# Kernel tuning notes

Hardware: AMD Instinct MI355X
Metric: run time of the kernel (lower is better)

The kernel has to match this reference:

```python
import jax, jax.numpy as jnp
import numpy as np

N_NODES = 15
K = 5
L_IN = 1920
C_OUT = 256
L3 = L_IN - 3 * K + 3  # 1908
EPS = 1e-5


def setup_inputs() -> dict:
    key = jax.random.key(0)
    ks = jax.random.split(key, 18)
    B, E = 128, 56
    s = 0.05
    inp = {
        'X': jax.random.normal(ks[0], (B, N_NODES, L_IN), jnp.float32),
        'edge_index': jax.random.randint(ks[1], (2, E), 0, N_NODES),
        'edge_weight': jax.random.uniform(ks[2], (E,), jnp.float32),
        # grouped conv params (groups = N_NODES): per-group channels 1->16->32->1
        'conv1_w': jax.random.normal(ks[3], (16 * N_NODES, 1, K), jnp.float32) * s,
        'conv1_b': jnp.zeros((16 * N_NODES,), jnp.float32),
        'conv2_w': jax.random.normal(ks[4], (32 * N_NODES, 16, K), jnp.float32) * s,
        'conv2_b': jnp.zeros((32 * N_NODES,), jnp.float32),
        'conv3_w': jax.random.normal(ks[5], (N_NODES, 32, K), jnp.float32) * s,
        'conv3_b': jnp.zeros((N_NODES,), jnp.float32),
        # GCNConv: lin weight [out,in] + bias
        'gcn_w': jax.random.normal(ks[6], (C_OUT, L3), jnp.float32) * s,
        'gcn_b': jnp.zeros((C_OUT,), jnp.float32),
        'lin1_w': jax.random.normal(ks[7], (C_OUT, L_IN), jnp.float32) * s,
        'lin1_b': jnp.zeros((C_OUT,), jnp.float32),
        # GraphNorm params
        'gn_w': jnp.ones((C_OUT,), jnp.float32),
        'gn_b': jnp.zeros((C_OUT,), jnp.float32),
        'gn_ms': jnp.ones((C_OUT,), jnp.float32),
        'out_w': jax.random.normal(ks[8], (16, C_OUT), jnp.float32) * s,
        'out_b': jnp.zeros((16,), jnp.float32),
    }
    return inp


def _gconv(x, w, b):
    # grouped valid conv1d, NCH layout
    y = jax.lax.conv_general_dilated(
        x, w, window_strides=(1,), padding='VALID',
        dimension_numbers=('NCH', 'OIH', 'NCH'),
        feature_group_count=N_NODES)
    return y + b[None, :, None]


def _gcn(x, edge_index, edge_weight, W, b):
    # x: [B, N, L3]; batched GCNConv with shared edge structure (no per-t loop)
    src, dst = edge_index[0], edge_index[1]
    loop = jnp.arange(N_NODES)
    src = jnp.concatenate([src, loop])
    dst = jnp.concatenate([dst, loop])
    ew = jnp.concatenate([edge_weight, jnp.ones((N_NODES,), edge_weight.dtype)])
    deg = jnp.zeros((N_NODES,), ew.dtype).at[dst].add(ew)  # in-degree on target
    dinv = jnp.where(deg > 0, jax.lax.rsqrt(deg), 0.0)
    norm = dinv[src] * ew * dinv[dst]  # [E']
    xl = jnp.einsum('bnf,of->bno', x, W)  # [B, N, C_OUT]
    msg = norm[None, :, None] * xl[:, src, :]  # [B, E', C_OUT]
    out = jnp.zeros_like(xl).at[:, dst, :].add(msg)
    return out + b


def reference(X, edge_index, edge_weight, conv1_w, conv1_b, conv2_w, conv2_b,
              conv3_w, conv3_b, gcn_w, gcn_b, lin1_w, lin1_b, gn_w, gn_b,
              gn_ms, out_w, out_b):
    h = jax.nn.leaky_relu(_gconv(X, conv1_w, conv1_b), 0.01)
    h = jax.nn.leaky_relu(_gconv(h, conv2_w, conv2_b), 0.01)
    h = jax.nn.leaky_relu(_gconv(h, conv3_w, conv3_b), 0.01)  # [B, N, L3]
    T = _gcn(h, edge_index, edge_weight, gcn_w, gcn_b)  # [B, N, C_OUT]
    # GraphNorm with batch=None -> single graph over dim 0
    mean = T.mean(axis=0, keepdims=True)
    out = T - mean * gn_ms
    var = (out * out).mean(axis=0, keepdims=True)
    T = gn_w * out / jnp.sqrt(var + EPS) + gn_b
    T = jax.nn.elu(T + jnp.einsum('bnl,ol->bno', X, lin1_w) + lin1_b)
    output = T.mean(axis=1)  # global_mean_pool over nodes -> [B, C_OUT]
    class_output = output @ out_w.T + out_b  # [B, 16]
    return (output, class_output)
```

## Files before the change

kernel.cpp:

```cpp
#include <hip/hip_runtime.h>

typedef unsigned short u16;
typedef unsigned int   u32;

typedef short shortx8  __attribute__((ext_vector_type(8)));
typedef float floatx4  __attribute__((ext_vector_type(4)));
typedef u32   uintx4   __attribute__((ext_vector_type(4)));

typedef u32     u32a     __attribute__((may_alias));
typedef uintx4  uintx4a  __attribute__((may_alias));
typedef shortx8 shortx8a __attribute__((may_alias));

__device__ __forceinline__ float bf2f(u16 u){
  union { u32 i; float f; } v; v.i = ((u32)u) << 16; return v.f;
}
__device__ __forceinline__ u16 f2bf(float f){
  union { float f; u32 i; } v; v.f = f;
  return (u16)((v.i + 0x7fffu + ((v.i >> 16) & 1u)) >> 16);
}
__device__ __forceinline__ u16 f2bf_fast(float f){
  union { float f; u32 i; } v; v.f = f;
  return (u16)((v.i + 0x8000u) >> 16);
}
__device__ __forceinline__ u32 pack2(float lo, float hi){
  union { float f; u32 i; } a, b; a.f = lo; b.f = hi;
  return __builtin_amdgcn_perm(b.i + 0x8000u, a.i + 0x8000u, 0x07060302u);
}
__device__ __forceinline__ float lrelu(float v){ return fmaxf(v, 0.01f*v); }

__global__ void __launch_bounds__(256) prep(const float* __restrict__ lw,
                                            u16* __restrict__ lwb,
                                            const float* __restrict__ gw,
                                            u16* __restrict__ gwp,
                                            float* __restrict__ zbase){
  const int b = blockIdx.x, tid = threadIdx.x;
  if (b < 480){
    const int base = b*1024 + tid;
    #pragma unroll
    for (int u = 0; u < 4; ++u) lwb[base + 256*u] = f2bf(lw[base + 256*u]);
  } else {
    const int row = b - 480;
    for (int col = tid; col < 1920; col += 256)
      gwp[row*1920 + col] = (col < 1908) ? f2bf(gw[row*1908 + col]) : (u16)0;
  }
  const int gidx = b*256 + tid;
  #pragma unroll
  for (int u = 0; u < 6; ++u){
    int i = gidx + u*188416;
    if (i < 983040) zbase[i] = 0.f;
  }
}

__global__ void __launch_bounds__(512, 4) fused_conv(
    const float* __restrict__ X,
    const float* __restrict__ w1, const float* __restrict__ b1,
    const float* __restrict__ w2, const float* __restrict__ b2,
    const float* __restrict__ w3, const float* __restrict__ b3,
    u16* __restrict__ h3p, u16* __restrict__ Xb){
  const int tid  = threadIdx.x;
  const int node = blockIdx.z;
  const int p    = blockIdx.x * 60;
  const int b0   = blockIdx.y * 16;

  __shared__ __attribute__((aligned(16))) u16 sH1[8*1632];
  __shared__ __attribute__((aligned(16))) u16 sH2[8*2720];
  __shared__ __attribute__((aligned(16))) u16 sW2f[3072];
  __shared__ __attribute__((aligned(16))) u16 sW3f[160];
  __shared__ u16 sXb[16*76];
  __shared__ float sW1[80], sB1[16], sB2[32];

  {
    const int bls = tid >> 5, i0 = tid & 31;
    const float* xrow = X  + (size_t)((b0 + bls)*15 + node)*1920;
    u16*        xbrow = Xb + (size_t)((b0 + bls)*15 + node)*1920;
    #pragma unroll
    for (int u = 0; u < 3; ++u){
      int i = i0 + 32*u;
      if (i < 76){
        int g = p + i;
        float xv = (i < 72 && g < 1920) ? xrow[g] : 0.f;
        u16 xb = f2bf_fast(xv);
        sXb[bls*76 + i] = xb;
        if (i < 60) xbrow[g] = xb;
      }
    }
    #pragma unroll
    for (int u = 0; u < 6; ++u){
      int d = tid + 512*u;
      int j = d & 7, mm = (d >> 3) & 15, qd = (d >> 7) & 3, t6 = d >> 9;
      int o = (t6 >= 3) ? 1 : 0, pi = t6 - 3*o;
      int tap = 2*pi + (qd >> 1), icc = (qd & 1)*8 + j, oc = o*16 + mm;
      sW2f[d] = (tap < 5) ? f2bf(w2[node*2560 + (oc*16 + icc)*5 + tap]) : (u16)0;
    }
    if (tid < 160){
      int icc = tid / 5, tp = tid - 5*icc;
      sW3f[tp*32 + icc] = f2bf(w3[node*160 + tid]);
    }
    if (tid < 80) sW1[tid] = w1[node*80 + tid];
    if (tid < 16) sB1[tid] = b1[node*16 + tid];
    if (tid < 32) sB2[tid] = b2[node*32 + tid];
  }
  __syncthreads();

  const int w = tid >> 6, lane = tid & 63;
  const int m = lane & 15, quad = lane >> 4;
  const int icb = (quad & 1)*8;
  const int tpo = quad >> 1;

  shortx8 a2[2][3];
  #pragma unroll
  for (int o = 0; o < 2; ++o)
    #pragma unroll
    for (int pi = 0; pi < 3; ++pi)
      a2[o][pi] = *(const shortx8a*)&sW2f[((o*3 + pi)*4 + quad)*128 + m*8];

  shortx8 a3[5];
  {
    const shortx8 zv = {0,0,0,0,0,0,0,0};
    #pragma unroll
    for (int tp = 0; tp < 5; ++tp){
      shortx8 t = *(const shortx8a*)&sW3f[tp*32 + quad*8];
      a3[tp] = (m == 0) ? t : zv;
    }
  }
  float biasr2[2][4];
  #pragma unroll
  for (int o = 0; o < 2; ++o)
    #pragma unroll
    for (int r = 0; r < 4; ++r)
      biasr2[o][r] = sB2[o*16 + quad*4 + r];
  const float b3v = b3[node];

  u16* h1w = sH1 + w*1632;
  u16* h2w = sH2 + w*2720;
  for (int i = lane; i < 160; i += 64) h2w[2560 + i] = 0;

  const int c1ic = (lane & 7)*2, c1t0 = (lane >> 3)*9;
  float wa[5], wb[5];
  #pragma unroll
  for (int k = 0; k < 5; ++k){ wa[k] = sW1[c1ic*5 + k]; wb[k] = sW1[c1ic*5 + 5 + k]; }
  const float ba = sB1[c1ic], bbv = sB1[c1ic + 1];

  for (int bb = 0; bb < 2; ++bb){
    const int bl = w + bb*8;

    {
      const u16* xr = sXb + bl*76;
      float x0 = bf2f(xr[c1t0]),   x1 = bf2f(xr[c1t0+1]);
      float x2 = bf2f(xr[c1t0+2]), x3 = bf2f(xr[c1t0+3]);
      #pragma unroll
      for (int i = 0; i < 9; ++i){
        const int t = c1t0 + i;
        float x4 = bf2f(xr[t + 4]);
        float va = ba  + wa[0]*x0 + wa[1]*x1 + wa[2]*x2 + wa[3]*x3 + wa[4]*x4;
        float vb = bbv + wb[0]*x0 + wb[1]*x1 + wb[2]*x2 + wb[3]*x3 + wb[4]*x4;
        va = lrelu(va); vb = lrelu(vb);
        if (t < 68) *(u32a*)(h1w + t*24 + c1ic) = pack2(va, vb);
        x0 = x1; x1 = x2; x2 = x3; x3 = x4;
      }
    }
    __syncthreads();

    #pragma unroll
    for (int q = 0; q < 4; ++q){
      const int trow = q*16 + m;
      shortx8 bf0 = *(const shortx8a*)(h1w + (trow     + tpo)*24 + icb);
      shortx8 bf1 = *(const shortx8a*)(h1w + (trow + 2 + tpo)*24 + icb);
      shortx8 bf2 = *(const shortx8a*)(h1w + (trow + 4      )*24 + icb);
      floatx4 ac0 = {0.f,0.f,0.f,0.f}, ac1 = {0.f,0.f,0.f,0.f};
      ac0 = __builtin_amdgcn_mfma_f32_16x16x32_bf16(a2[0][0], bf0, ac0, 0, 0, 0);
      ac1 = __builtin_amdgcn_mfma_f32_16x16x32_bf16(a2[1][0], bf0, ac1, 0, 0, 0);
      ac0 = __builtin_amdgcn_mfma_f32_16x16x32_bf16(a2[0][1], bf1, ac0, 0, 0, 0);
      ac1 = __builtin_amdgcn_mfma_f32_16x16x32_bf16(a2[1][1], bf1, ac1, 0, 0, 0);
      ac0 = __builtin_amdgcn_mfma_f32_16x16x32_bf16(a2[0][2], bf2, ac0, 0, 0, 0);
      ac1 = __builtin_amdgcn_mfma_f32_16x16x32_bf16(a2[1][2], bf2, ac1, 0, 0, 0);
      #pragma unroll
      for (int o = 0; o < 2; ++o){
        const floatx4& ac = o ? ac1 : ac0;
        float v0 = lrelu(ac[0] + biasr2[o][0]);
        float v1 = lrelu(ac[1] + biasr2[o][1]);
        float v2 = lrelu(ac[2] + biasr2[o][2]);
        float v3 = lrelu(ac[3] + biasr2[o][3]);
        u16* dst = h2w + trow*40 + o*16 + quad*4;
        *(u32a*)(dst)     = pack2(v0, v1);
        *(u32a*)(dst + 2) = pack2(v2, v3);
      }
    }
    __syncthreads();

    const int rg = (b0 + bl)*15 + node;
    #pragma unroll
    for (int nt = 0; nt < 4; ++nt){
      floatx4 acc3 = {0.f,0.f,0.f,0.f};
      if (lane < 16) acc3[0] = b3v;
      #pragma unroll
      for (int tp = 0; tp < 5; ++tp){
        shortx8 bfr = *(const shortx8a*)(h2w + (nt*16 + m + tp)*40 + quad*8);
        acc3 = __builtin_amdgcn_mfma_f32_16x16x32_bf16(a3[tp], bfr, acc3, 0, 0, 0);
      }
      const int tl = nt*16 + lane;
      if (lane < 16 && tl < 60){
        const int t3 = p + tl;
        float v = lrelu(acc3[0]);
        h3p[(size_t)rg*1920 + t3] = (t3 < 1908) ? f2bf_fast(v) : (u16)0;
      }
    }
  }
}

__global__ void __launch_bounds__(256) gemm_nt(
    const u16* __restrict__ A0, const u16* __restrict__ B0, float* __restrict__ O0,
    const u16* __restrict__ A1, const u16* __restrict__ B1, float* __restrict__ O1){
  const int job = blockIdx.z >> 1, kh = blockIdx.z & 1;
  const u16* A; const u16* Bm; float* O;
  if (job == 0){ A = A0; Bm = B0; O = O0; } else { A = A1; Bm = B1; O = O1; }
  __shared__ __attribute__((aligned(16))) u16 sA[64*88];
  __shared__ __attribute__((aligned(16))) u16 sB[64*88];
  const int tid = threadIdx.x;
  const int m0 = blockIdx.x*64, n0 = blockIdx.y*64;
  const int row = tid >> 2, kc = tid & 3;
  const int w = tid >> 6, lane = tid & 63;
  const int m = lane & 15, quad = lane >> 4;
  const int mo = (w & 1)*32, no = (w >> 1)*32;
  floatx4 acc[2][2];
  #pragma unroll
  for (int i = 0; i < 2; ++i)
    #pragma unroll
    for (int j = 0; j < 2; ++j)
      #pragma unroll
      for (int r = 0; r < 4; ++r) acc[i][j][r] = 0.f;

  const u16* ap = A  + (size_t)(m0 + row)*1920 + kh*960 + kc*8;
  const u16* bp = Bm + (size_t)(n0 + row)*1920 + kh*960 + kc*8;
  for (int kt = 0; kt < 15; ++kt){
    uintx4 va0 = *(const uintx4a*)ap;
    uintx4 va1 = *(const uintx4a*)(ap + 32);
    uintx4 vb0 = *(const uintx4a*)bp;
    uintx4 vb1 = *(const uintx4a*)(bp + 32);
    ap += 64; bp += 64;
    *(uintx4a*)&sA[row*88 + kc*8]      = va0;
    *(uintx4a*)&sA[row*88 + 32 + kc*8] = va1;
    *(uintx4a*)&sB[row*88 + kc*8]      = vb0;
    *(uintx4a*)&sB[row*88 + 32 + kc*8] = vb1;
    __syncthreads();
    #pragma unroll
    for (int ks = 0; ks < 64; ks += 32){
      const shortx8 af0 = *(const shortx8a*)&sA[(mo      + m)*88 + ks + quad*8];
      const shortx8 af1 = *(const shortx8a*)&sA[(mo + 16 + m)*88 + ks + quad*8];
      const shortx8 bf0 = *(const shortx8a*)&sB[(no      + m)*88 + ks + quad*8];
      const shortx8 bf1 = *(const shortx8a*)&sB[(no + 16 + m)*88 + ks + quad*8];
      acc[0][0] = __builtin_amdgcn_mfma_f32_16x16x32_bf16(af0, bf0, acc[0][0], 0, 0, 0);
      acc[0][1] = __builtin_amdgcn_mfma_f32_16x16x32_bf16(af0, bf1, acc[0][1], 0, 0, 0);
      acc[1][0] = __builtin_amdgcn_mfma_f32_16x16x32_bf16(af1, bf0, acc[1][0], 0, 0, 0);
      acc[1][1] = __builtin_amdgcn_mfma_f32_16x16x32_bf16(af1, bf1, acc[1][1], 0, 0, 0);
    }
    __syncthreads();
  }
  #pragma unroll
  for (int mi = 0; mi < 2; ++mi)
    #pragma unroll
    for (int ni = 0; ni < 2; ++ni)
      #pragma unroll
      for (int r = 0; r < 4; ++r){
        int rr = m0 + mo + mi*16 + quad*4 + r;
        int cc = n0 + no + ni*16 + m;
        atomicAdd(&O[(size_t)rr*256 + cc], acc[mi][ni][r]);
      }
}

__global__ void __launch_bounds__(256) gcn_agg(
    const float* __restrict__ xl, const int* __restrict__ ei,
    const float* __restrict__ ew, const float* __restrict__ gcn_b,
    float* __restrict__ Tpre){
  const int b = blockIdx.x, tid = threadIdx.x;
  __shared__ float sxl[15*256];
  __shared__ float s_deg[15], s_dinv[15], s_norm[71];
  __shared__ int   s_cnt[15], s_start[16], s_fill[15], s_srcl[71];
  if (tid < 15){ s_deg[tid] = 0.f; s_cnt[tid] = 0; s_fill[tid] = 0; }
  #pragma unroll
  for (int n = 0; n < 15; ++n)
    sxl[n*256 + tid] = xl[(size_t)(b*15 + n)*256 + tid];
  __syncthreads();
  int se = 0, de = 0; float we = 0.f;
  if (tid < 71){
    if (tid < 56){ se = ei[tid]; de = ei[56 + tid]; we = ew[tid]; }
    else         { se = tid - 56; de = tid - 56; we = 1.0f; }
    atomicAdd(&s_deg[de], we);
    atomicAdd(&s_cnt[de], 1);
  }
  __syncthreads();
  if (tid < 15) s_dinv[tid] = s_deg[tid] > 0.f ? rsqrtf(s_deg[tid]) : 0.f;
  if (tid == 0){
    int a = 0;
    for (int n = 0; n < 15; ++n){ s_start[n] = a; a += s_cnt[n]; }
    s_start[15] = a;
  }
  __syncthreads();
  if (tid < 71){
    float nrm = s_dinv[se]*we*s_dinv[de];
    int pos = s_start[de] + atomicAdd(&s_fill[de], 1);
    s_srcl[pos] = se; s_norm[pos] = nrm;
  }
  __syncthreads();
  const float gb = gcn_b[tid];
  for (int n = 0; n < 15; ++n){
    float acc = gb;
    const int e0 = s_start[n], e1 = s_start[n+1];
    for (int idx = e0; idx < e1; ++idx)
      acc += s_norm[idx]*sxl[s_srcl[idx]*256 + tid];
    Tpre[(size_t)(b*15 + n)*256 + tid] = acc;
  }
}

__global__ void __launch_bounds__(256) gn_stats(
    const float* __restrict__ Tpre, const float* __restrict__ gn_ms,
    const float* __restrict__ gn_w, float* __restrict__ moff, float* __restrict__ scal){
  const int n = blockIdx.x, c = threadIdx.x;
  float s = 0.f, s2 = 0.f;
  for (int b = 0; b < 128; ++b){
    float v = Tpre[(size_t)(b*15 + n)*256 + c];
    s += v; s2 += v*v;
  }
  const float mean = s*(1.f/128.f);
  const float mo = mean*gn_ms[c];
  float var = s2*(1.f/128.f) - 2.f*mo*mean + mo*mo;
  var = fmaxf(var, 0.f);
  moff[n*256 + c] = mo;
  scal[n*256 + c] = gn_w[c]*rsqrtf(var + 1e-5f);
}

__global__ void __launch_bounds__(256) finalize_k(
    const float* __restrict__ Tpre, const float* __restrict__ l1,
    const float* __restrict__ moff, const float* __restrict__ scal,
    const float* __restrict__ gn_b, const float* __restrict__ lin1_b,
    const float* __restrict__ out_w, const float* __restrict__ out_b,
    float* __restrict__ dout){
  const int b = blockIdx.x, tid = threadIdx.x;
  __shared__ float spool[256], spart[256];
  const float gnb = gn_b[tid], lb = lin1_b[tid];
  float acc = 0.f;
  #pragma unroll
  for (int n = 0; n < 15; ++n){
    float t = (Tpre[(size_t)(b*15 + n)*256 + tid] - moff[n*256 + tid])*scal[n*256 + tid]
              + gnb + l1[(size_t)(b*15 + n)*256 + tid] + lb;
    t = t > 0.f ? t : (__expf(t) - 1.f);
    acc += t;
  }
  const float pool = acc*(1.f/15.f);
  dout[b*256 + tid] = pool;
  spool[tid] = pool;
  __syncthreads();
  const int j = tid >> 4, q = tid & 15;
  float s = 0.f;
  for (int i = 0; i < 16; ++i){
    int cc = q + i*16;
    s += spool[cc]*out_w[j*256 + cc];
  }
  spart[tid] = s;
  __syncthreads();
  if (tid < 16){
    float tot = out_b[tid];
    #pragma unroll
    for (int i = 0; i < 16; ++i) tot += spart[tid*16 + i];
    dout[32768 + b*16 + tid] = tot;
  }
}

extern "C" void kernel_launch(void* const* d_in, const int* in_sizes, int n_in,
                              void* d_out, int out_size, void* d_ws, size_t ws_size,
                              hipStream_t stream){
  (void)in_sizes; (void)n_in; (void)out_size; (void)ws_size;
  const float* X    = (const float*)d_in[0];
  const int*   ei   = (const int*)d_in[1];
  const float* ew   = (const float*)d_in[2];
  const float* w1   = (const float*)d_in[3];
  const float* b1   = (const float*)d_in[4];
  const float* w2   = (const float*)d_in[5];
  const float* b2   = (const float*)d_in[6];
  const float* w3   = (const float*)d_in[7];
  const float* b3   = (const float*)d_in[8];
  const float* gw   = (const float*)d_in[9];
  const float* gb   = (const float*)d_in[10];
  const float* lw   = (const float*)d_in[11];
  const float* lb   = (const float*)d_in[12];
  const float* gnw  = (const float*)d_in[13];
  const float* gnb  = (const float*)d_in[14];
  const float* gnms = (const float*)d_in[15];
  const float* ow   = (const float*)d_in[16];
  const float* ob   = (const float*)d_in[17];

  char* ws = (char*)d_ws;
  u16*   h3p  = (u16*)(ws + 0);
  u16*   gwp  = (u16*)(ws + 7372800);
  u16*   Xb   = (u16*)(ws + 8355840);
  u16*   lwb  = (u16*)(ws + 15728640);
  float* xl   = (float*)(ws + 16711680);
  float* l1   = (float*)(ws + 18677760);
  float* Tpre = (float*)(ws + 0);
  float* moff = (float*)(ws + 7372800);
  float* scal = (float*)(ws + 7388160);

  prep      <<<dim3(736),        dim3(256), 0, stream>>>(lw, lwb, gw, gwp,
                                                         (float*)(ws + 16711680));
  fused_conv<<<dim3(32, 8, 15),  dim3(512), 0, stream>>>(X, w1, b1, w2, b2, w3, b3,
                                                         h3p, Xb);
  gemm_nt   <<<dim3(30, 4, 4),   dim3(256), 0, stream>>>(Xb, lwb, l1, h3p, gwp, xl);
  gcn_agg   <<<dim3(128),        dim3(256), 0, stream>>>(xl, ei, ew, gb, Tpre);
  gn_stats  <<<dim3(15),         dim3(256), 0, stream>>>(Tpre, gnms, gnw, moff, scal);
  finalize_k<<<dim3(128),        dim3(256), 0, stream>>>(Tpre, l1, moff, scal,
                                                         gnb, lb, ow, ob, (float*)d_out);
}
```

Measured before the change: 219.4 us.

## Fold prep into conv, switch conv2 to 32x32 MFMA, fuse GraphNorm stats

Removes the prep kernel by having fused_conv blocks also convert lin1 and gcn weights to bf16. Conv2 moves from 16x16x32 MFMAs to 32x32x16 MFMAs over five taps, with a repacked weight layout and the bias folded into the accumulator init. The GEMM drops its K split and atomics in favour of plain stores. GraphNorm sum and sum-of-squares are now accumulated with atomics inside gcn_agg and turned into scales in finalize, which removes the gn_stats kernel. Together this cuts two launches, at the cost of extra atomic traffic and fewer GEMM blocks.

```diff
diff --git a/kernel.cpp b/kernel.cpp
--- a/kernel.cpp
+++ b/kernel.cpp
@@ -3,17 +3,15 @@
 typedef unsigned short u16;
 typedef unsigned int   u32;
 
-typedef short shortx8  __attribute__((ext_vector_type(8)));
-typedef float floatx4  __attribute__((ext_vector_type(4)));
-typedef u32   uintx4   __attribute__((ext_vector_type(4)));
+typedef short shortx8   __attribute__((ext_vector_type(8)));
+typedef float floatx4   __attribute__((ext_vector_type(4)));
+typedef float floatx16  __attribute__((ext_vector_type(16)));
+typedef u32   uintx4    __attribute__((ext_vector_type(4)));
 
 typedef u32     u32a     __attribute__((may_alias));
 typedef uintx4  uintx4a  __attribute__((may_alias));
 typedef shortx8 shortx8a __attribute__((may_alias));
 
-__device__ __forceinline__ float bf2f(u16 u){
-  union { u32 i; float f; } v; v.i = ((u32)u) << 16; return v.f;
-}
 __device__ __forceinline__ u16 f2bf(float f){
   union { float f; u32 i; } v; v.f = f;
   return (u16)((v.i + 0x7fffu + ((v.i >> 16) & 1u)) >> 16);
@@ -26,37 +24,28 @@
   union { float f; u32 i; } a, b; a.f = lo; b.f = hi;
   return __builtin_amdgcn_perm(b.i + 0x8000u, a.i + 0x8000u, 0x07060302u);
 }
+__device__ __forceinline__ u32 cvtpk2(float lo, float hi){
+#if __has_builtin(__builtin_amdgcn_cvt_pk_bf16_f32)
+  auto pv = __builtin_amdgcn_cvt_pk_bf16_f32(lo, hi);
+  if constexpr (sizeof(pv) == 4){
+    u32 out; __builtin_memcpy(&out, &pv, 4); return out;
+  } else {
+    return pack2(lo, hi);
+  }
+#else
+  return pack2(lo, hi);
+#endif
+}
 __device__ __forceinline__ float lrelu(float v){ return fmaxf(v, 0.01f*v); }
-
-__global__ void __launch_bounds__(256) prep(const float* __restrict__ lw,
-                                            u16* __restrict__ lwb,
-                                            const float* __restrict__ gw,
-                                            u16* __restrict__ gwp,
-                                            float* __restrict__ zbase){
-  const int b = blockIdx.x, tid = threadIdx.x;
-  if (b < 480){
-    const int base = b*1024 + tid;
-    #pragma unroll
-    for (int u = 0; u < 4; ++u) lwb[base + 256*u] = f2bf(lw[base + 256*u]);
-  } else {
-    const int row = b - 480;
-    for (int col = tid; col < 1920; col += 256)
-      gwp[row*1920 + col] = (col < 1908) ? f2bf(gw[row*1908 + col]) : (u16)0;
-  }
-  const int gidx = b*256 + tid;
-  #pragma unroll
-  for (int u = 0; u < 6; ++u){
-    int i = gidx + u*188416;
-    if (i < 983040) zbase[i] = 0.f;
-  }
-}
 
 __global__ void __launch_bounds__(512, 4) fused_conv(
     const float* __restrict__ X,
     const float* __restrict__ w1, const float* __restrict__ b1,
     const float* __restrict__ w2, const float* __restrict__ b2,
     const float* __restrict__ w3, const float* __restrict__ b3,
-    u16* __restrict__ h3p, u16* __restrict__ Xb){
+    u16* __restrict__ h3p, u16* __restrict__ Xb,
+    const float* __restrict__ lw, u16* __restrict__ lwb,
+    const float* __restrict__ gw, u16* __restrict__ gwp){
   const int tid  = threadIdx.x;
   const int node = blockIdx.z;
   const int p    = blockIdx.x * 60;
@@ -64,10 +53,25 @@
 
   __shared__ __attribute__((aligned(16))) u16 sH1[8*1632];
   __shared__ __attribute__((aligned(16))) u16 sH2[8*2720];
-  __shared__ __attribute__((aligned(16))) u16 sW2f[3072];
+  __shared__ __attribute__((aligned(16))) u16 sW2f[2560];
   __shared__ __attribute__((aligned(16))) u16 sW3f[160];
   __shared__ u16 sXb[16*76];
   __shared__ float sW1[80], sB1[16], sB2[32];
+
+  {
+    const int bid = blockIdx.x + 32*(blockIdx.y + 8*blockIdx.z);
+    if (tid < 256){
+      int gid = bid*256 + tid;
+      if (gid < 491520){
+        lwb[gid] = f2bf(lw[gid]);
+      } else {
+        int g2 = gid - 491520;
+        int row = g2 / 1920;
+        int col = g2 - row*1920;
+        gwp[g2] = (col < 1908) ? f2bf(gw[row*1908 + col]) : (u16)0;
+      }
+    }
+  }
 
   {
     const int bls = tid >> 5, i0 = tid & 31;
@@ -85,12 +89,10 @@
       }
     }
     #pragma unroll
-    for (int u = 0; u < 6; ++u){
+    for (int u = 0; u < 5; ++u){
       int d = tid + 512*u;
-      int j = d & 7, mm = (d >> 3) & 15, qd = (d >> 7) & 3, t6 = d >> 9;
-      int o = (t6 >= 3) ? 1 : 0, pi = t6 - 3*o;
-      int tap = 2*pi + (qd >> 1), icc = (qd & 1)*8 + j, oc = o*16 + mm;
-      sW2f[d] = (tap < 5) ? f2bf(w2[node*2560 + (oc*16 + icc)*5 + tap]) : (u16)0;
+      int j = d & 7, oc = (d >> 3) & 31, h = (d >> 8) & 1, tap = d >> 9;
+      sW2f[d] = f2bf(w2[node*2560 + (oc*16 + h*8 + j)*5 + tap]);
     }
     if (tid < 160){
       int icc = tid / 5, tp = tid - 5*icc;
@@ -104,15 +106,17 @@
 
   const int w = tid >> 6, lane = tid & 63;
   const int m = lane & 15, quad = lane >> 4;
-  const int icb = (quad & 1)*8;
-  const int tpo = quad >> 1;
-
-  shortx8 a2[2][3];
-  #pragma unroll
-  for (int o = 0; o < 2; ++o)
-    #pragma unroll
-    for (int pi = 0; pi < 3; ++pi)
-      a2[o][pi] = *(const shortx8a*)&sW2f[((o*3 + pi)*4 + quad)*128 + m*8];
+  const int t32 = lane & 31, h = lane >> 5;
+
+  shortx8 a2t[5];
+  #pragma unroll
+  for (int tap = 0; tap < 5; ++tap)
+    a2t[tap] = *(const shortx8a*)&sW2f[((tap*2 + h)*32 + t32)*8];
+
+  float biasr[16];
+  #pragma unroll
+  for (int r = 0; r < 16; ++r)
+    biasr[r] = sB2[(r&3) + 8*(r>>2) + 4*h];
 
   shortx8 a3[5];
   {
@@ -123,12 +127,6 @@
       a3[tp] = (m == 0) ? t : zv;
     }
   }
-  float biasr2[2][4];
-  #pragma unroll
-  for (int o = 0; o < 2; ++o)
-    #pragma unroll
-    for (int r = 0; r < 4; ++r)
-      biasr2[o][r] = sB2[o*16 + quad*4 + r];
   const float b3v = b3[node];
 
   u16* h1w = sH1 + w*1632;
@@ -146,44 +144,41 @@
 
     {
       const u16* xr = sXb + bl*76;
-      float x0 = bf2f(xr[c1t0]),   x1 = bf2f(xr[c1t0+1]);
-      float x2 = bf2f(xr[c1t0+2]), x3 = bf2f(xr[c1t0+3]);
+      union { u32 i; float f; } cv;
+      float xw[5];
+      #pragma unroll
+      for (int k = 0; k < 4; ++k){ cv.i = ((u32)xr[c1t0+k]) << 16; xw[k] = cv.f; }
       #pragma unroll
       for (int i = 0; i < 9; ++i){
         const int t = c1t0 + i;
-        float x4 = bf2f(xr[t + 4]);
-        float va = ba  + wa[0]*x0 + wa[1]*x1 + wa[2]*x2 + wa[3]*x3 + wa[4]*x4;
-        float vb = bbv + wb[0]*x0 + wb[1]*x1 + wb[2]*x2 + wb[3]*x3 + wb[4]*x4;
+        cv.i = ((u32)xr[t + 4]) << 16; xw[4] = cv.f;
+        float va = ba  + wa[0]*xw[0] + wa[1]*xw[1] + wa[2]*xw[2] + wa[3]*xw[3] + wa[4]*xw[4];
+        float vb = bbv + wb[0]*xw[0] + wb[1]*xw[1] + wb[2]*xw[2] + wb[3]*xw[3] + wb[4]*xw[4];
         va = lrelu(va); vb = lrelu(vb);
-        if (t < 68) *(u32a*)(h1w + t*24 + c1ic) = pack2(va, vb);
-        x0 = x1; x1 = x2; x2 = x3; x3 = x4;
+        if (t < 68) *(u32a*)(h1w + t*24 + c1ic) = cvtpk2(va, vb);
+        xw[0] = xw[1]; xw[1] = xw[2]; xw[2] = xw[3]; xw[3] = xw[4];
       }
     }
     __syncthreads();
 
     #pragma unroll
-    for (int q = 0; q < 4; ++q){
-      const int trow = q*16 + m;
-      shortx8 bf0 = *(const shortx8a*)(h1w + (trow     + tpo)*24 + icb);
-      shortx8 bf1 = *(const shortx8a*)(h1w + (trow + 2 + tpo)*24 + icb);
-      shortx8 bf2 = *(const shortx8a*)(h1w + (trow + 4      )*24 + icb);
-      floatx4 ac0 = {0.f,0.f,0.f,0.f}, ac1 = {0.f,0.f,0.f,0.f};
-      ac0 = __builtin_amdgcn_mfma_f32_16x16x32_bf16(a2[0][0], bf0, ac0, 0, 0, 0);
-      ac1 = __builtin_amdgcn_mfma_f32_16x16x32_bf16(a2[1][0], bf0, ac1, 0, 0, 0);
-      ac0 = __builtin_amdgcn_mfma_f32_16x16x32_bf16(a2[0][1], bf1, ac0, 0, 0, 0);
-      ac1 = __builtin_amdgcn_mfma_f32_16x16x32_bf16(a2[1][1], bf1, ac1, 0, 0, 0);
-      ac0 = __builtin_amdgcn_mfma_f32_16x16x32_bf16(a2[0][2], bf2, ac0, 0, 0, 0);
-      ac1 = __builtin_amdgcn_mfma_f32_16x16x32_bf16(a2[1][2], bf2, ac1, 0, 0, 0);
-      #pragma unroll
-      for (int o = 0; o < 2; ++o){
-        const floatx4& ac = o ? ac1 : ac0;
-        float v0 = lrelu(ac[0] + biasr2[o][0]);
-        float v1 = lrelu(ac[1] + biasr2[o][1]);
-        float v2 = lrelu(ac[2] + biasr2[o][2]);
-        float v3 = lrelu(ac[3] + biasr2[o][3]);
-        u16* dst = h2w + trow*40 + o*16 + quad*4;
-        *(u32a*)(dst)     = pack2(v0, v1);
-        *(u32a*)(dst + 2) = pack2(v2, v3);
+    for (int nt = 0; nt < 2; ++nt){
+      const int t0 = nt*32;
+      floatx16 acc;
+      #pragma unroll
+      for (int r = 0; r < 16; ++r) acc[r] = biasr[r];
+      #pragma unroll
+      for (int tap = 0; tap < 5; ++tap){
+        shortx8 bfr = *(const shortx8a*)(h1w + (t0 + t32 + tap)*24 + h*8);
+        acc = __builtin_amdgcn_mfma_f32_32x32x16_bf16(a2t[tap], bfr, acc, 0, 0, 0);
+      }
+      u16* dst = h2w + (t0 + t32)*40;
+      #pragma unroll
+      for (int r = 0; r < 16; r += 2){
+        float v0 = lrelu(acc[r]);
+        float v1 = lrelu(acc[r+1]);
+        const int oc0 = (r&3) + 8*(r>>2) + 4*h;
+        *(u32a*)(dst + oc0) = cvtpk2(v0, v1);
       }
     }
     __syncthreads();
@@ -210,13 +205,18 @@
 
 __global__ void __launch_bounds__(256) gemm_nt(
     const u16* __restrict__ A0, const u16* __restrict__ B0, float* __restrict__ O0,
-    const u16* __restrict__ A1, const u16* __restrict__ B1, float* __restrict__ O1){
-  const int job = blockIdx.z >> 1, kh = blockIdx.z & 1;
+    const u16* __restrict__ A1, const u16* __restrict__ B1, float* __restrict__ O1,
+    float* __restrict__ gZ){
+  const int job = blockIdx.z;
   const u16* A; const u16* Bm; float* O;
   if (job == 0){ A = A0; Bm = B0; O = O0; } else { A = A1; Bm = B1; O = O1; }
   __shared__ __attribute__((aligned(16))) u16 sA[64*88];
   __shared__ __attribute__((aligned(16))) u16 sB[64*88];
   const int tid = threadIdx.x;
+  if (blockIdx.x == 0 && blockIdx.y == 0 && job == 0){
+    #pragma unroll
+    for (int u = 0; u < 30; ++u) gZ[tid + 256*u] = 0.f;
+  }
   const int m0 = blockIdx.x*64, n0 = blockIdx.y*64;
   const int row = tid >> 2, kc = tid & 3;
   const int w = tid >> 6, lane = tid & 63;
@@ -230,9 +230,9 @@
       #pragma unroll
       for (int r = 0; r < 4; ++r) acc[i][j][r] = 0.f;
 
-  const u16* ap = A  + (size_t)(m0 + row)*1920 + kh*960 + kc*8;
-  const u16* bp = Bm + (size_t)(n0 + row)*1920 + kh*960 + kc*8;
-  for (int kt = 0; kt < 15; ++kt){
+  const u16* ap = A  + (size_t)(m0 + row)*1920 + kc*8;
+  const u16* bp = Bm + (size_t)(n0 + row)*1920 + kc*8;
+  for (int kt = 0; kt < 30; ++kt){
     uintx4 va0 = *(const uintx4a*)ap;
     uintx4 va1 = *(const uintx4a*)(ap + 32);
     uintx4 vb0 = *(const uintx4a*)bp;
@@ -264,14 +264,14 @@
       for (int r = 0; r < 4; ++r){
         int rr = m0 + mo + mi*16 + quad*4 + r;
         int cc = n0 + no + ni*16 + m;
-        atomicAdd(&O[(size_t)rr*256 + cc], acc[mi][ni][r]);
+        O[(size_t)rr*256 + cc] = acc[mi][ni][r];
       }
 }
 
 __global__ void __launch_bounds__(256) gcn_agg(
     const float* __restrict__ xl, const int* __restrict__ ei,
     const float* __restrict__ ew, const float* __restrict__ gcn_b,
-    float* __restrict__ Tpre){
+    float* __restrict__ Tpre, float* __restrict__ gS, float* __restrict__ gS2){
   const int b = blockIdx.x, tid = threadIdx.x;
   __shared__ float sxl[15*256];
   __shared__ float s_deg[15], s_dinv[15], s_norm[71];
@@ -309,39 +309,33 @@
     for (int idx = e0; idx < e1; ++idx)
       acc += s_norm[idx]*sxl[s_srcl[idx]*256 + tid];
     Tpre[(size_t)(b*15 + n)*256 + tid] = acc;
-  }
-}
-
-__global__ void __launch_bounds__(256) gn_stats(
-    const float* __restrict__ Tpre, const float* __restrict__ gn_ms,
-    const float* __restrict__ gn_w, float* __restrict__ moff, float* __restrict__ scal){
-  const int n = blockIdx.x, c = threadIdx.x;
-  float s = 0.f, s2 = 0.f;
-  for (int b = 0; b < 128; ++b){
-    float v = Tpre[(size_t)(b*15 + n)*256 + c];
-    s += v; s2 += v*v;
-  }
-  const float mean = s*(1.f/128.f);
-  const float mo = mean*gn_ms[c];
-  float var = s2*(1.f/128.f) - 2.f*mo*mean + mo*mo;
-  var = fmaxf(var, 0.f);
-  moff[n*256 + c] = mo;
-  scal[n*256 + c] = gn_w[c]*rsqrtf(var + 1e-5f);
+    atomicAdd(&gS [n*256 + tid], acc);
+    atomicAdd(&gS2[n*256 + tid], acc*acc);
+  }
 }
 
 __global__ void __launch_bounds__(256) finalize_k(
     const float* __restrict__ Tpre, const float* __restrict__ l1,
-    const float* __restrict__ moff, const float* __restrict__ scal,
+    const float* __restrict__ gS, const float* __restrict__ gS2,
+    const float* __restrict__ gn_ms, const float* __restrict__ gn_w,
     const float* __restrict__ gn_b, const float* __restrict__ lin1_b,
     const float* __restrict__ out_w, const float* __restrict__ out_b,
     float* __restrict__ dout){
   const int b = blockIdx.x, tid = threadIdx.x;
   __shared__ float spool[256], spart[256];
   const float gnb = gn_b[tid], lb = lin1_b[tid];
+  const float gms = gn_ms[tid], gwc = gn_w[tid];
   float acc = 0.f;
   #pragma unroll
   for (int n = 0; n < 15; ++n){
-    float t = (Tpre[(size_t)(b*15 + n)*256 + tid] - moff[n*256 + tid])*scal[n*256 + tid]
+    const float s  = gS [n*256 + tid];
+    const float s2 = gS2[n*256 + tid];
+    const float mean = s*(1.f/128.f);
+    const float mo   = mean*gms;
+    float var = s2*(1.f/128.f) - 2.f*mo*mean + mo*mo;
+    var = fmaxf(var, 0.f);
+    const float scal = gwc*rsqrtf(var + 1e-5f);
+    float t = (Tpre[(size_t)(b*15 + n)*256 + tid] - mo)*scal
               + gnb + l1[(size_t)(b*15 + n)*256 + tid] + lb;
     t = t > 0.f ? t : (__expf(t) - 1.f);
     acc += t;
@@ -396,17 +390,15 @@
   u16*   lwb  = (u16*)(ws + 15728640);
   float* xl   = (float*)(ws + 16711680);
   float* l1   = (float*)(ws + 18677760);
+  float* gS   = (float*)(ws + 20643840);
+  float* gS2  = (float*)(ws + 20659200);
   float* Tpre = (float*)(ws + 0);
-  float* moff = (float*)(ws + 7372800);
-  float* scal = (float*)(ws + 7388160);
-
-  prep      <<<dim3(736),        dim3(256), 0, stream>>>(lw, lwb, gw, gwp,
-                                                         (float*)(ws + 16711680));
-  fused_conv<<<dim3(32, 8, 15),  dim3(512), 0, stream>>>(X, w1, b1, w2, b2, w3, b3,
-                                                         h3p, Xb);
-  gemm_nt   <<<dim3(30, 4, 4),   dim3(256), 0, stream>>>(Xb, lwb, l1, h3p, gwp, xl);
-  gcn_agg   <<<dim3(128),        dim3(256), 0, stream>>>(xl, ei, ew, gb, Tpre);
-  gn_stats  <<<dim3(15),         dim3(256), 0, stream>>>(Tpre, gnms, gnw, moff, scal);
-  finalize_k<<<dim3(128),        dim3(256), 0, stream>>>(Tpre, l1, moff, scal,
-                                                         gnb, lb, ow, ob, (float*)d_out);
-}
+
+  fused_conv<<<dim3(32, 8, 15), dim3(512), 0, stream>>>(X, w1, b1, w2, b2, w3, b3,
+                                                        h3p, Xb, lw, lwb, gw, gwp);
+  gemm_nt   <<<dim3(30, 4, 2),  dim3(256), 0, stream>>>(Xb, lwb, l1, h3p, gwp, xl, gS);
+  gcn_agg   <<<dim3(128),       dim3(256), 0, stream>>>(xl, ei, ew, gb, Tpre, gS, gS2);
+  finalize_k<<<dim3(128),       dim3(256), 0, stream>>>(Tpre, l1, gS, gS2,
+                                                        gnms, gnw, gnb, lb, ow, ob,
+                                                        (float*)d_out);
+}
```

After: 205.5 us. 1.07x faster.
